# Performance work log

Hardware: AMD Instinct MI355X
Metric: run time of the kernel (lower is better)

The kernel has to match this reference:

```python
import jax, jax.numpy as jnp
import numpy as np
from jax import lax

B, N, FIN, T, K, FC, FT = 8, 2048, 3, 12, 3, 64, 64


def _conv2d(x, w, b, pad):
    # x [B,C,N,T], w [O,I,1,kw], NCHW conv
    y = lax.conv_general_dilated(x, w, (1, 1), pad,
                                 dimension_numbers=('NCHW', 'OIHW', 'NCHW'))
    return y + b[None, :, None, None]


def _spatial_att(h, W, a, alpha, concat):
    # GAT-style dense attention. h [B,N,Fin], W [Fin,D], a [2D,1]
    D = W.shape[1]
    Wh = h @ W                                             # [B,N,D]
    e = jax.nn.leaky_relu(Wh @ a[:D] + jnp.swapaxes(Wh @ a[D:], 1, 2), alpha)  # [B,N,N]
    att = jax.nn.softmax(jax.nn.sigmoid(e), axis=1)        # softmax over dim=1 (as in torch)
    hp = jnp.einsum('bij,bjd->bid', att, Wh)
    return jax.nn.elu(hp) if concat else hp


def setup_inputs() -> dict:
    key = jax.random.key(0)
    ks = jax.random.split(key, 24)
    rnd = lambda i, shape, scale=1.0: (jax.random.normal(ks[i], shape, dtype=jnp.float32) * scale)
    FTm = FC * T  # 768 spatial-attention feature dim
    D = FTm // 2
    return {
        'x': rnd(0, (B, N, FIN, T)),
        'cheb': rnd(1, (K, N, N), 1.0 / np.sqrt(N)),
        'Gamma': rnd(2, (K, FIN, FC), 1.0 / np.sqrt(FIN)),
        'W_heads': rnd(3, (2, FTm, D), 1.0 / np.sqrt(FTm)),
        'a_heads': rnd(4, (2, 2 * D, 1), 1.0 / np.sqrt(2 * D)),
        'W_out': rnd(5, (FTm, FTm), 1.0 / np.sqrt(FTm)),
        'a_out': rnd(6, (2 * FTm, 1), 1.0 / np.sqrt(2 * FTm)),
        'U1': rnd(7, (FT, FT), 1.0 / np.sqrt(FT)),
        'U2': rnd(8, (FT,), 1.0 / np.sqrt(FT)),
        'U3': rnd(9, (FT,), 1.0 / np.sqrt(FT)),
        'be': rnd(10, (1, T, T), 0.1),
        'Ve': rnd(11, (T, T), 1.0 / np.sqrt(T)),
        'time_w': rnd(12, (FT, FC, 1, 3), 1.0 / np.sqrt(3 * FC)),
        'time_b': rnd(13, (FT,), 0.01),
        'res_w': rnd(14, (FT, FIN, 1, 1), 1.0 / np.sqrt(FIN)),
        'res_b': rnd(15, (FT,), 0.01),
        'back_w': rnd(16, (FT, FC, 1, 3), 1.0 / np.sqrt(3 * FC)),
        'back_b': rnd(17, (FT,), 0.01),
        'fore_w': rnd(18, (FT, FC, 1, 3), 1.0 / np.sqrt(3 * FC)),
        'fore_b': rnd(19, (FT,), 0.01),
        'ln_g': jnp.ones((FT,), jnp.float32),
        'ln_b': jnp.zeros((FT,), jnp.float32),
    }


def reference(x, cheb, Gamma, W_heads, a_heads, W_out, a_out, U1, U2, U3, be, Ve,
              time_w, time_b, res_w, res_b, back_w, back_b, fore_w, fore_b, ln_g, ln_b):
    b, n, fin, t = x.shape
    k_ = cheb.shape[0]
    fc = Gamma.shape[2]
    # ChebNetII interpolation coefficients T_k(x_j), x_j = cos((j+0.5)pi/K) -> [j,k]
    jj = np.arange(k_)
    cxj = jnp.asarray(np.cos(np.outer((jj + 0.5) * np.pi / k_, np.arange(k_))), x.dtype)
    lhs = jnp.einsum('jio,jk->kio', Gamma, cxj)                         # [K,Fin,Fc]
    rhs = jnp.einsum('bnit,knm->kbmit', x, cheb)                        # [K,B,N,Fin,T]
    spatial_gcn = jax.nn.relu((2.0 / (k_ + 1)) * jnp.einsum('kbmit,kio->bmot', rhs, lhs))  # [B,N,Fc,T]

    # Spatial transformer: 2 GAT heads + output attention
    h = spatial_gcn.reshape(b, n, fc * t)
    heads = jax.vmap(lambda W, a: _spatial_att(h, W, a, 0.1, True))(W_heads, a_heads)  # [H,B,N,D]
    hcat = jnp.transpose(heads, (1, 2, 0, 3)).reshape(b, n, -1)
    gcn_SAt = jax.nn.relu(_spatial_att(hcat, W_out, a_out, 0.1, False)).reshape(b, n, fc, t)

    # Temporal conv (1x3, pad 1)
    tc = _conv2d(jnp.transpose(gcn_SAt, (0, 2, 1, 3)), time_w, time_b, ((0, 0), (1, 1)))
    tc = jnp.transpose(tc, (0, 2, 1, 3))                                # [B,N,Ft,T]

    # Temporal attention
    lhs_t = jnp.einsum('bnft,fg,g->btn', tc, U1, U2)                    # [B,T,N]
    rhs_t = jnp.einsum('f,bnft->bnt', U3, tc)                           # [B,N,T]
    prod = jnp.einsum('bsn,bnt->bst', lhs_t, rhs_t)                     # [B,T,T]
    E = jnp.einsum('is,bst->bit', Ve, jax.nn.sigmoid(prod + be))
    E = jax.nn.softmax(E, axis=1)
    tcn = jnp.einsum('bnft,bts->bnfs', tc, E)                           # [B,N,Ft,T]

    # Residual (1x1 conv) + LayerNorm over channel dim
    x_res = _conv2d(jnp.transpose(x, (0, 2, 1, 3)), res_w, res_b, ((0, 0), (0, 0)))
    x_res = jnp.transpose(x_res, (0, 2, 1, 3))                          # [B,N,Ft,T]
    z = jnp.transpose(jax.nn.relu(x_res + tcn), (0, 3, 1, 2))           # [B,T,N,Ft]
    mu = z.mean(-1, keepdims=True)
    var = z.var(-1, keepdims=True)
    z = (z - mu) / jnp.sqrt(var + 1e-5) * ln_g + ln_b
    result = jnp.transpose(z, (0, 2, 3, 1))                             # [B,N,Ft,T]

    rp = jnp.transpose(result, (0, 2, 1, 3))
    backcast = jnp.transpose(_conv2d(rp, back_w, back_b, ((0, 0), (1, 1))), (0, 2, 1, 3))
    forecast = jnp.transpose(_conv2d(rp, fore_w, fore_b, ((0, 0), (1, 1))), (0, 2, 1, 3))
    return (backcast, forecast)
```

## Files before the change

kernel.cpp:

```cpp
#include <hip/hip_runtime.h>


typedef unsigned short u16;
typedef __bf16 bf16x8 __attribute__((ext_vector_type(8)));
typedef float f32x4 __attribute__((ext_vector_type(4)));
typedef u16 u16x8 __attribute__((ext_vector_type(8)));

__device__ __forceinline__ u16 f2b(float f) {
  union { float f; unsigned u; } v; v.f = f;
  unsigned u = v.u;
  u = u + 0x7FFFu + ((u >> 16) & 1u);
  return (u16)(u >> 16);
}
__device__ __forceinline__ float b2f(u16 h) {
  union { unsigned u; float f; } v; v.u = ((unsigned)h) << 16; return v.f;
}
__device__ __forceinline__ float qfun(float x) {
  float e = x > 0.f ? x : 0.1f * x;
  float s = __builtin_amdgcn_rcpf(1.f + __expf(-e));
  return __expf(s);
}

template <int N> __device__ __forceinline__ void waitvm() {
  if constexpr (N == 0)      asm volatile("s_waitcnt vmcnt(0)" ::: "memory");
  else if constexpr (N == 4) asm volatile("s_waitcnt vmcnt(4)" ::: "memory");
  else                       asm volatile("s_waitcnt vmcnt(6)" ::: "memory");
}
__device__ __forceinline__ void rawbar() { asm volatile("s_barrier" ::: "memory"); }

#define GLOAD16(g, l) __builtin_amdgcn_global_load_lds( \
    (__attribute__((address_space(1))) void*)(g),       \
    (__attribute__((address_space(3))) void*)(l), 16, 0, 0)

constexpr size_t OFF_LHS     = 0x0;
constexpr size_t OFF_U1U2    = 0x1000;
constexpr size_t OFF_BIASBIG = 0x1100;
constexpr size_t OFF_FH      = 0x3000;
constexpr size_t OFF_GH      = 0x23000;
constexpr size_t OFF_RDH     = 0x43000;
constexpr size_t OFF_FO      = 0x63000;
constexpr size_t OFF_GO      = 0x73000;
constexpr size_t OFF_RDO     = 0x83000;
constexpr size_t OFF_LHST    = 0x93000;
constexpr size_t OFF_RHST    = 0x153000;
constexpr size_t OFF_PROD    = 0x213000;
constexpr size_t OFF_E       = 0x215000;
constexpr size_t OFF_WCATT   = 0x220000;
constexpr size_t OFF_WOUTT   = 0x340000;
constexpr size_t OFF_WTBIG   = 0x460000;
constexpr size_t OFF_XCOLT   = 0x580000;
constexpr size_t OFF_CHEBT   = 0x700000;
constexpr size_t OFF_C1      = 0x1F00000;
constexpr size_t OFF_H       = 0x4300000;
constexpr size_t OFF_P       = 0x700000;
constexpr size_t OFF_WHCATT  = 0x5B00000;
constexpr size_t OFF_HCAT    = 0x7300000;
constexpr size_t OFF_WHOUTT  = 0x5B00000;
constexpr size_t OFF_GCNB    = 0x7300000;
constexpr size_t OFF_WBFBIG  = 0x8B00000;
constexpr size_t OFF_TCS     = 0x700000;
constexpr size_t OFF_RESULTB = 0x3700000;
constexpr size_t WS_NEEDED   = 0x8D40000;

struct GemmP {
  const u16* A; const u16* BT;
  long sA, sB;
  int K, lda, ldb;
  int swz, splitK;
  float* Cf; long sCf; int ldcf;
  u16* Cb;  long sCb; int ldcb;
  u16* CbT; int ldcT; long sCbT;
  const float* bias;
  float* outB; float* outF;
};

template <int EPI, int WN>
__global__ __launch_bounds__(256, (WN == 1 ? 3 : 2)) void gemm_bf16(GemmP p) {
  constexpr int BUFU  = (WN == 1) ? 8192 : 12288;
  constexpr int SMEMU = (WN == 1) ? 16384 : 24576;
  constexpr int LPW   = (WN == 1) ? 4 : 6;
  __shared__ u16 smem[SMEMU];
  const int tid  = threadIdx.x;
  const int lane = tid & 63;
  const int wid  = tid >> 6;
  const int wm = wid >> 1, wn = wid & 1;
  const int z = blockIdx.z;

  long m0, n0;
  if (p.swz) {
    int nT = gridDim.x;
    int nwg = nT * gridDim.y;
    int lin = blockIdx.x + nT * blockIdx.y;
    int q = nwg >> 3;
    int swz = (lin & 7) * q + (lin >> 3);
    m0 = (long)(swz / nT) * 128;
    n0 = (long)(swz % nT) * (128 * WN);
  } else {
    m0 = (long)blockIdx.y * 128;
    n0 = (long)blockIdx.x * (128 * WN);
  }

  const int K = p.K;
  long aBase, bBase;
  if (p.splitK) {
    int kz = z >> 2, ch = z & 3;
    aBase = (long)kz * p.sA + (long)ch * 512;
    bBase = (long)ch * 512;
  } else {
    aBase = (long)z * p.sA;
    bBase = (long)z * p.sB;
  }
  const u16* Ab = p.A + aBase + m0 * p.lda;
  const u16* Bb = p.BT + bBase + n0 * p.ldb;

  const int sk = (((lane & 3) ^ ((lane >> 3) & 3))) * 8;
  const u16* aP0 = Ab + (long)(wid * 32 + (lane >> 2)) * p.lda + sk;
  const u16* aP1 = aP0 + (long)16 * p.lda;
  const u16* bP0 = Bb + (long)(wid * 32 * WN + (lane >> 2)) * p.ldb + sk;
  const u16* bP1 = bP0 + (long)16 * p.ldb;
  const u16* bP2 = bP0 + (long)32 * p.ldb;
  const u16* bP3 = bP0 + (long)48 * p.ldb;
  const int aslot = wid * 1024;
  const int bslot = 4096 + wid * (WN == 1 ? 1024 : 2048);

  auto STAGE = [&](int s, u16* base) {
    long ko = (long)s * 32;
    GLOAD16(aP0 + ko, base + aslot);
    GLOAD16(aP1 + ko, base + aslot + 512);
    GLOAD16(bP0 + ko, base + bslot);
    GLOAD16(bP1 + ko, base + bslot + 512);
    if constexpr (WN == 2) {
      GLOAD16(bP2 + ko, base + bslot + 1024);
      GLOAD16(bP3 + ko, base + bslot + 1536);
    }
  };

  f32x4 acc[4][4 * WN];
  f32x4 zero = {0.f, 0.f, 0.f, 0.f};
#pragma unroll
  for (int i = 0; i < 4; ++i)
#pragma unroll
    for (int j = 0; j < 4 * WN; ++j) acc[i][j] = zero;

  const int xorc = (lane >> 1) & 3;
  const int aoff = (wm * 64 + (lane & 15)) * 32 + ((lane >> 4) ^ xorc) * 8;
  const int boff = 4096 + (wn * 64 * WN + (lane & 15)) * 32 + ((lane >> 4) ^ xorc) * 8;

  const int nsteps = K >> 5;
  u16* buf0 = smem;
  u16* buf1 = smem + BUFU;

  STAGE(0, buf0);
  STAGE(1, buf1);
  waitvm<LPW>();
  rawbar();

  for (int i = 0; i < nsteps; ++i) {
    u16* buf = (i & 1) ? buf1 : buf0;
    bf16x8 av[4], bv[4 * WN];
#pragma unroll
    for (int mi = 0; mi < 4; ++mi) av[mi] = *(const bf16x8*)&buf[aoff + mi * 512];
#pragma unroll
    for (int ni = 0; ni < 4 * WN; ++ni) bv[ni] = *(const bf16x8*)&buf[boff + ni * 512];
#pragma unroll
    for (int mi = 0; mi < 4; ++mi)
#pragma unroll
      for (int ni = 0; ni < 4 * WN; ++ni)
        acc[mi][ni] = __builtin_amdgcn_mfma_f32_16x16x32_bf16(av[mi], bv[ni], acc[mi][ni], 0, 0, 0);
    if (i + 1 < nsteps) {
      asm volatile("s_waitcnt lgkmcnt(0)" ::: "memory");
      rawbar();
      if (i + 2 < nsteps) {
        STAGE(i + 2, buf);
        waitvm<LPW>();
      } else {
        waitvm<0>();
      }
      rawbar();
    }
  }
  __syncthreads();

  if constexpr (EPI == 1) {
#pragma unroll
    for (int h = 0; h < 2; ++h) {
      if (h == 1) __syncthreads();
      if (WN == 1 || wn == h) {
#pragma unroll
        for (int mi = 0; mi < 4; ++mi)
#pragma unroll
          for (int ni = 0; ni < 4 * WN; ++ni) {
            int cl = (WN == 1 ? wn * 64 : 0) + ni * 16 + (lane & 15);
            int mlb = wm * 64 + mi * 16 + ((lane >> 4) << 2);
#pragma unroll
            for (int r = 0; r < 4; ++r)
              smem[cl * 136 + mlb + r] = f2b(acc[mi][ni][r]);
          }
      }
      __syncthreads();
      int c = tid >> 1, half = tid & 1;
      long bat = m0 >> 11;
      u16* dst = p.CbT + bat * p.sCbT + (long)(n0 + h * 128 + c) * p.ldcT +
                 (m0 & 2047) + half * 64;
      const u16* srcp = &smem[c * 136 + half * 64];
#pragma unroll
      for (int j = 0; j < 64; j += 8)
        *(u16x8*)(dst + j) = *(const u16x8*)(srcp + j);
      if (WN == 1) break;
    }
    return;
  }

  if constexpr (EPI == 7) {
    const int q = lane >> 4, g4 = (lane >> 2) & 3, j = lane & 3;
    const int back = ((int)n0 < 768);
    float* obase = (back ? p.outB : p.outF) - (back ? 0 : 768);
#pragma unroll
    for (int mi = 0; mi < 4; ++mi) {
      long rb0 = m0 + wm * 64 + mi * 16 + q * 4;
#pragma unroll
      for (int ni = 0; ni < 4 * WN; ++ni) {
        int cb = (int)n0 + wn * 64 * WN + ni * 16 + g4 * 4;
        f32x4 v = acc[mi][ni];
        float bsv = p.bias[cb + j];
        v[0] += bsv; v[1] += bsv; v[2] += bsv; v[3] += bsv;
#pragma unroll
        for (int d = 1; d <= 2; d <<= 1) {
          f32x4 t;
#pragma unroll
          for (int b = 0; b < 4; ++b) t[b] = __shfl_xor(v[b ^ d], d, 64);
#pragma unroll
          for (int b = 0; b < 4; ++b) if ((lane ^ b) & d) v[b] = t[b];
        }
        *(f32x4*)(obase + (rb0 + j) * 768 + cb) = v;
      }
    }
    return;
  }

#pragma unroll
  for (int mi = 0; mi < 4; ++mi) {
    long rb0 = m0 + wm * 64 + mi * 16 + ((lane >> 4) << 2);
#pragma unroll
    for (int ni = 0; ni < 4 * WN; ++ni) {
      int col = (int)n0 + wn * 64 * WN + ni * 16 + (lane & 15);
#pragma unroll
      for (int r = 0; r < 4; ++r) {
        float v = acc[mi][ni][r];
        long row = rb0 + r;
        if constexpr (EPI == 2) {
          float e = v > 0.f ? v : expm1f(v);
          p.Cb[(long)z * p.sCb + row * p.ldcb + col] = f2b(e);
        } else if constexpr (EPI == 6) {
          p.Cb[row * 768 + col] = f2b(v + p.bias[col & 63]);
        } else if constexpr (EPI == 9) {
          p.Cb[(long)z * p.sCb + row * p.ldcb + col] = f2b(v);
        } else {
          p.Cb[(long)z * p.sCb + row * p.ldcb + col] = f2b(fmaxf(v, 0.f));
        }
      }
    }
  }
}

__global__ void k_prep(const float* Gamma, const float* U1, const float* U2,
                       const float* back_b, const float* fore_b,
                       float* lhs, float* u1u2, float* biasBig) {
  int o = threadIdx.x;
  if (o < 64) {
    const float cx[3][3] = {{1.f, 0.86602540378443871f, 0.5f},
                            {1.f, 6.123233995736766e-17f, -1.f},
                            {1.f, -0.86602540378443871f, 0.5f}};
    for (int k = 0; k < 3; ++k)
      for (int i = 0; i < 3; ++i) {
        float s = 0;
        for (int j = 0; j < 3; ++j) s += Gamma[(j * 3 + i) * 64 + o] * cx[j][k];
        lhs[(k * 3 + i) * 64 + o] = s;
      }
    float s = 0;
    for (int g = 0; g < 64; ++g) s += U1[o * 64 + g] * U2[g];
    u1u2[o] = s;
    for (int t = 0; t < 12; ++t) {
      biasBig[o * 12 + t] = back_b[o];
      biasBig[768 + o * 12 + t] = fore_b[o];
    }
  }
}

__global__ void k_convert(const float* W_heads, const float* W_out, const float* time_w,
                          const float* back_w, const float* fore_w, const float* xg,
                          u16* WcatT, u16* WoutT, u16* WtBig, u16* WbfBig, u16* xcolT) {
  const int N1 = 589824, NT = 589824, NBF = 1179648, N5 = 786432;
  const int TOT = 2 * N1 + NT + NBF + N5;
  for (int o = blockIdx.x * 256 + threadIdx.x; o < TOT; o += gridDim.x * 256) {
    if (o < N1) {
      int dcol = o / 768, kk = o % 768;
      int hd = dcol / 384, d = dcol % 384;
      WcatT[o] = f2b(W_heads[((long)hd * 768 + kk) * 384 + d]);
    } else if (o < 2 * N1) {
      int o2 = o - N1; int dcol = o2 / 768, kk = o2 % 768;
      WoutT[o2] = f2b(W_out[kk * 768 + dcol]);
    } else if (o < 2 * N1 + NT) {
      int o3 = o - 2 * N1; int col = o3 / 768, kk = o3 % 768;
      int t = col >> 6, ft = col & 63, fc = kk / 12, tau = kk % 12;
      int r = tau - t + 1;
      WtBig[o3] = f2b((r >= 0 && r < 3) ? time_w[ft * 192 + fc * 3 + r] : 0.f);
    } else if (o < 2 * N1 + NT + NBF) {
      int o4 = o - 2 * N1 - NT; int col = o4 / 768, kk = o4 % 768;
      int rem = (col < 768) ? col : col - 768;
      int c = rem / 12, tt = rem % 12;
      int fc = kk / 12, tau = kk % 12; int r = tau - tt + 1;
      const float* wsrc = (col < 768) ? back_w : fore_w;
      WbfBig[o4] = f2b((r >= 0 && r < 3) ? wsrc[c * 192 + fc * 3 + r] : 0.f);
    } else {
      int o5 = o - 2 * N1 - NT - NBF; int c = o5 / 2048, n = o5 % 2048;
      float v = 0.f;
      if (c < 288) {
        int b = c / 36, r2 = c % 36, i = r2 / 12, t = r2 % 12;
        v = xg[(long)(b * 2048 + n) * 36 + i * 12 + t];
      }
      xcolT[o5] = f2b(v);
    }
  }
}

__global__ void k_chebT(const float* cheb, u16* chebT) {
  __shared__ float ts[32][33];
  int n0 = blockIdx.x * 32, m0 = blockIdx.y * 32, k = blockIdx.z;
  int c = threadIdx.x & 31, rq = threadIdx.x >> 5;
  const long base = (long)k * 2048 * 2048;
  for (int q = 0; q < 4; ++q) {
    int n = n0 + rq + q * 8;
    ts[rq + q * 8][c] = cheb[base + (long)n * 2048 + m0 + c];
  }
  __syncthreads();
  for (int q = 0; q < 4; ++q) {
    int m = m0 + rq + q * 8;
    chebT[base + (long)m * 2048 + n0 + c] = f2b(ts[c][rq + q * 8]);
  }
}

__global__ __launch_bounds__(256) void k_h(const u16* C1, const float* lhs, u16* h) {
  int bn = blockIdx.x; int b = bn >> 11, n = bn & 2047;
  int tid = threadIdx.x;
  __shared__ float c1s[108], ls[576];
  if (tid < 108) {
    int kk = tid / 12, t = tid % 12; int k = kk / 3, i = kk % 3;
    float s = 0;
#pragma unroll
    for (int ch = 0; ch < 4; ++ch)
      s += b2f(C1[((long)(k * 4 + ch) * 2048 + n) * 384 + b * 36 + i * 12 + t]);
    c1s[tid] = s;
  }
  for (int s = tid; s < 576; s += 256) ls[s] = lhs[s];
  __syncthreads();
  for (int q = 0; q < 3; ++q) {
    int idx = tid + q * 256; int o = idx / 12, t = idx % 12;
    float s = 0;
#pragma unroll
    for (int kk = 0; kk < 9; ++kk) s += c1s[kk * 12 + t] * ls[kk * 64 + o];
    s *= 0.5f;
    if (s < 0.f) s = 0.f;
    h[(long)bn * 768 + idx] = f2b(s);
  }
}

__global__ __launch_bounds__(256) void k_fg(const u16* WhT, int dOff, int Dlen,
                                            const float* aF, const float* aG,
                                            float* fOut, float* gOut) {
  int b = blockIdx.y;
  int i = blockIdx.x * 256 + threadIdx.x;
  __shared__ float af[768], ag[768];
  for (int s = threadIdx.x; s < Dlen; s += 256) { af[s] = aF[s]; ag[s] = aG[s]; }
  __syncthreads();
  const u16* wp = WhT + ((long)b * 768 + dOff) * 2048 + i;
  float fs = 0, gs = 0;
  for (int d = 0; d < Dlen; ++d) {
    float w = b2f(wp[(long)d * 2048]);
    fs += w * af[d]; gs += w * ag[d];
  }
  fOut[b * 2048 + i] = fs;
  gOut[b * 2048 + i] = gs;
}

__global__ __launch_bounds__(256) void k_denom(const float* f, const float* g, float* rd) {
  int b = blockIdx.y;
  int jl = threadIdx.x & 63, ch = threadIdx.x >> 6;
  int j = blockIdx.x * 64 + jl;
  __shared__ float fl[2048];
  __shared__ float red[256];
  for (int s = threadIdx.x; s < 2048; s += 256) fl[s] = f[b * 2048 + s];
  __syncthreads();
  float gj = g[b * 2048 + j];
  float acc = 0;
  for (int i = ch * 512; i < ch * 512 + 512; ++i) acc += qfun(fl[i] + gj);
  red[threadIdx.x] = acc;
  __syncthreads();
  if (ch == 0) {
    float s = red[jl] + red[jl + 64] + red[jl + 128] + red[jl + 192];
    rd[b * 2048 + j] = 1.f / s;
  }
}

__global__ __launch_bounds__(256) void k_P(const float* f, const float* g,
                                           const float* rd, u16* P) {
  int j = blockIdx.x * 256 + threadIdx.x;
  int i0 = blockIdx.y * 16;
  int b = blockIdx.z;
  __shared__ float fl[16];
  if (threadIdx.x < 16) fl[threadIdx.x] = f[b * 2048 + i0 + threadIdx.x];
  __syncthreads();
  float gj = g[b * 2048 + j], rj = rd[b * 2048 + j];
  u16* Pp = P + ((long)b * 2048 + i0) * 2048 + j;
#pragma unroll
  for (int ii = 0; ii < 16; ++ii) Pp[(long)ii * 2048] = f2b(qfun(fl[ii] + gj) * rj);
}

__global__ void k_temporal(const u16* tc, const float* u1u2, const float* U3g,
                           float* lhs_t, float* rhs_t) {
  __shared__ float uu[64], u3[64];
  int tid = threadIdx.x;
  if (tid < 64) { uu[tid] = u1u2[tid]; u3[tid] = U3g[tid]; }
  __syncthreads();
  int gid = blockIdx.x * 256 + tid;
  const u16* p = tc + (long)gid * 64;
  float s1 = 0, s2 = 0;
#pragma unroll
  for (int c = 0; c < 8; ++c) {
    u16x8 vv = *(const u16x8*)(p + c * 8);
#pragma unroll
    for (int j = 0; j < 8; ++j) {
      float v = b2f(vv[j]);
      s1 += v * uu[c * 8 + j]; s2 += v * u3[c * 8 + j];
    }
  }
  int t = gid % 12; long bn = gid / 12;
  int b = (int)(bn >> 11);
  lhs_t[((long)b * 12 + t) * 2048 + (int)(bn & 2047)] = s1;
  rhs_t[gid] = s2;
}

__global__ void k_prod(const float* lhs_t, const float* rhs_t, float* prod) {
  int bi = blockIdx.x;
  int b = bi / 144; int r = bi % 144; int s = r / 12; int u = r % 12;
  int tid = threadIdx.x;
  float acc = 0;
  const float* lp = lhs_t + ((long)b * 12 + s) * 2048;
  const float* rp = rhs_t + (long)b * 2048 * 12 + u;
  for (int n = tid; n < 2048; n += 256) acc += lp[n] * rp[n * 12];
  __shared__ float red[256];
  red[tid] = acc; __syncthreads();
  for (int st = 128; st > 0; st >>= 1) {
    if (tid < st) red[tid] += red[tid + st];
    __syncthreads();
  }
  if (tid == 0) prod[bi] = red[0];
}

__global__ void k_E(const float* prod, const float* be, const float* Ve, float* E) {
  int b = blockIdx.x; int tid = threadIdx.x;
  __shared__ float S0[144], E1[144], mx[12], dn[12];
  if (tid < 144) {
    float v = prod[b * 144 + tid] + be[tid];
    S0[tid] = 1.f / (1.f + __expf(-v));
  }
  __syncthreads();
  if (tid < 144) {
    int i = tid / 12, t = tid % 12;
    float a = 0;
    for (int s = 0; s < 12; ++s) a += Ve[i * 12 + s] * S0[s * 12 + t];
    E1[tid] = a;
  }
  __syncthreads();
  if (tid < 12) {
    float m = -1e30f;
    for (int i = 0; i < 12; ++i) m = fmaxf(m, E1[i * 12 + tid]);
    float d = 0;
    for (int i = 0; i < 12; ++i) d += __expf(E1[i * 12 + tid] - m);
    mx[tid] = m; dn[tid] = d;
  }
  __syncthreads();
  if (tid < 144) {
    int t = tid % 12;
    E[b * 144 + tid] = __expf(E1[tid] - mx[t]) / dn[t];
  }
}

__global__ __launch_bounds__(256) void k_res_ln(const u16* tc, const float* E,
                                                const float* xg, const float* res_w,
                                                const float* res_b, const float* ln_g,
                                                const float* ln_b, u16* result) {
  int bn = blockIdx.x; int b = bn >> 11;
  int tid = threadIdx.x;
  __shared__ float tcb[768], Eb[144], xl[36], rw[192], rb[64], lg[64], lb[64], zl[768], mu[12], rs[12];
  for (int s = tid; s < 768; s += 256) tcb[s] = b2f(tc[(long)bn * 768 + s]);
  if (tid < 144) Eb[tid] = E[b * 144 + tid];
  if (tid < 36) xl[tid] = xg[(long)bn * 36 + tid];
  if (tid >= 64 && tid < 256) { int q = tid - 64; if (q < 192) rw[q] = res_w[q]; }
  if (tid < 64) { rb[tid] = res_b[tid]; lg[tid] = ln_g[tid]; lb[tid] = ln_b[tid]; }
  __syncthreads();
  float z[3];
#pragma unroll
  for (int q = 0; q < 3; ++q) {
    int idx = tid + q * 256; int f = idx / 12, s = idx % 12;
    float tcn = 0;
#pragma unroll
    for (int t = 0; t < 12; ++t) tcn += tcb[t * 64 + f] * Eb[t * 12 + s];
    float xr = rb[f];
#pragma unroll
    for (int i = 0; i < 3; ++i) xr += rw[f * 3 + i] * xl[i * 12 + s];
    float v = xr + tcn;
    v = v > 0.f ? v : 0.f;
    z[q] = v; zl[idx] = v;
  }
  __syncthreads();
  if (tid < 12) {
    float m = 0, m2 = 0;
    for (int f = 0; f < 64; ++f) { float v = zl[f * 12 + tid]; m += v; m2 += v * v; }
    m *= (1.f / 64.f); m2 *= (1.f / 64.f);
    mu[tid] = m;
    float var = m2 - m * m;
    rs[tid] = rsqrtf((var > 0.f ? var : 0.f) + 1e-5f);
  }
  __syncthreads();
#pragma unroll
  for (int q = 0; q < 3; ++q) {
    int idx = tid + q * 256; int f = idx / 12, s = idx % 12;
    result[(long)bn * 768 + idx] = f2b((z[q] - mu[s]) * rs[s] * lg[f] + lb[f]);
  }
}

__global__ void k_sentinel(float* out, long n) {
  long i = (long)blockIdx.x * 256 + threadIdx.x;
  if (i < n) out[i] = 12345.0f;
}

extern "C" void kernel_launch(void* const* d_in, const int* in_sizes, int n_in,
                              void* d_out, int out_size, void* d_ws, size_t ws_size,
                              hipStream_t stream) {
  (void)in_sizes; (void)n_in;
  const float* x       = (const float*)d_in[0];
  const float* cheb    = (const float*)d_in[1];
  const float* Gamma   = (const float*)d_in[2];
  const float* W_heads = (const float*)d_in[3];
  const float* a_heads = (const float*)d_in[4];
  const float* W_out   = (const float*)d_in[5];
  const float* a_out   = (const float*)d_in[6];
  const float* U1      = (const float*)d_in[7];
  const float* U2      = (const float*)d_in[8];
  const float* U3      = (const float*)d_in[9];
  const float* be      = (const float*)d_in[10];
  const float* Ve      = (const float*)d_in[11];
  const float* time_w  = (const float*)d_in[12];
  const float* time_b  = (const float*)d_in[13];
  const float* res_w   = (const float*)d_in[14];
  const float* res_b   = (const float*)d_in[15];
  const float* back_w  = (const float*)d_in[16];
  const float* back_b  = (const float*)d_in[17];
  const float* fore_w  = (const float*)d_in[18];
  const float* fore_b  = (const float*)d_in[19];
  const float* ln_g    = (const float*)d_in[20];
  const float* ln_b    = (const float*)d_in[21];
  float* out = (float*)d_out;

  if (ws_size < WS_NEEDED) {
    k_sentinel<<<(out_size + 255) / 256, 256, 0, stream>>>(out, out_size);
    return;
  }

  char* ws = (char*)d_ws;
  float* lhs     = (float*)(ws + OFF_LHS);
  float* u1u2    = (float*)(ws + OFF_U1U2);
  float* biasBig = (float*)(ws + OFF_BIASBIG);
  float* fH      = (float*)(ws + OFF_FH);
  float* gH      = (float*)(ws + OFF_GH);
  float* rdH     = (float*)(ws + OFF_RDH);
  float* fO      = (float*)(ws + OFF_FO);
  float* gO      = (float*)(ws + OFF_GO);
  float* rdO     = (float*)(ws + OFF_RDO);
  float* lhs_t   = (float*)(ws + OFF_LHST);
  float* rhs_t   = (float*)(ws + OFF_RHST);
  float* prod    = (float*)(ws + OFF_PROD);
  float* Ebuf    = (float*)(ws + OFF_E);
  u16* WcatT   = (u16*)(ws + OFF_WCATT);
  u16* WoutT   = (u16*)(ws + OFF_WOUTT);
  u16* WtBig   = (u16*)(ws + OFF_WTBIG);
  u16* WbfBig  = (u16*)(ws + OFF_WBFBIG);
  u16* xcolT   = (u16*)(ws + OFF_XCOLT);
  u16* chebT   = (u16*)(ws + OFF_CHEBT);
  u16* C1      = (u16*)(ws + OFF_C1);
  u16* hbuf    = (u16*)(ws + OFF_H);
  u16* Pbuf    = (u16*)(ws + OFF_P);
  u16* WhcatT  = (u16*)(ws + OFF_WHCATT);
  u16* hcat    = (u16*)(ws + OFF_HCAT);
  u16* WhoutT  = (u16*)(ws + OFF_WHOUTT);
  u16* gcnB    = (u16*)(ws + OFF_GCNB);
  u16* tcsB    = (u16*)(ws + OFF_TCS);
  u16* resultB = (u16*)(ws + OFF_RESULTB);

  k_prep<<<1, 64, 0, stream>>>(Gamma, U1, U2, back_b, fore_b, lhs, u1u2, biasBig);
  k_convert<<<2048, 256, 0, stream>>>(W_heads, W_out, time_w, back_w, fore_w, x,
                                      WcatT, WoutT, WtBig, WbfBig, xcolT);
  k_chebT<<<dim3(64, 64, 3), 256, 0, stream>>>(cheb, chebT);

  {
    GemmP p{}; p.A = chebT; p.BT = xcolT; p.sA = 2048L * 2048; p.sB = 0;
    p.K = 512; p.lda = 2048; p.ldb = 2048; p.splitK = 1; p.swz = 1;
    p.Cb = C1; p.sCb = 2048L * 384; p.ldcb = 384;
    gemm_bf16<9, 1><<<dim3(3, 16, 12), 256, 0, stream>>>(p);
  }
  k_h<<<16384, 256, 0, stream>>>(C1, lhs, hbuf);

  {
    GemmP p{}; p.A = hbuf; p.BT = WcatT; p.sA = 0; p.sB = 0;
    p.K = 768; p.lda = 768; p.ldb = 768; p.swz = 1;
    p.CbT = WhcatT; p.ldcT = 2048; p.sCbT = 768L * 2048;
    gemm_bf16<1, 2><<<dim3(3, 128, 1), 256, 0, stream>>>(p);
  }
  k_fg<<<dim3(8, 8), 256, 0, stream>>>(WhcatT, 0, 384, a_heads, a_heads + 384, fH, gH);
  k_fg<<<dim3(8, 8), 256, 0, stream>>>(WhcatT, 384, 384, a_heads + 768, a_heads + 1152,
                                       fH + 16384, gH + 16384);
  for (int hd = 0; hd < 2; ++hd) {
    const float* f = fH + hd * 16384; const float* g = gH + hd * 16384;
    float* rd = rdH + hd * 16384;
    k_denom<<<dim3(32, 8), 256, 0, stream>>>(f, g, rd);
    k_P<<<dim3(8, 128, 8), 256, 0, stream>>>(f, g, rd, Pbuf);
    GemmP p{}; p.A = Pbuf; p.BT = WhcatT + (long)hd * 384 * 2048;
    p.sA = 2048L * 2048; p.sB = 768L * 2048;
    p.K = 2048; p.lda = 2048; p.ldb = 2048; p.swz = 1;
    p.Cb = hcat + hd * 384; p.sCb = 2048L * 768; p.ldcb = 768;
    gemm_bf16<2, 1><<<dim3(3, 16, 8), 256, 0, stream>>>(p);
  }

  {
    GemmP p{}; p.A = hcat; p.BT = WoutT; p.sA = 0; p.sB = 0;
    p.K = 768; p.lda = 768; p.ldb = 768; p.swz = 1;
    p.CbT = WhoutT; p.ldcT = 2048; p.sCbT = 768L * 2048;
    gemm_bf16<1, 2><<<dim3(3, 128, 1), 256, 0, stream>>>(p);
  }
  k_fg<<<dim3(8, 8), 256, 0, stream>>>(WhoutT, 0, 768, a_out, a_out + 768, fO, gO);
  k_denom<<<dim3(32, 8), 256, 0, stream>>>(fO, gO, rdO);
  k_P<<<dim3(8, 128, 8), 256, 0, stream>>>(fO, gO, rdO, Pbuf);
  {
    GemmP p{}; p.A = Pbuf; p.BT = WhoutT; p.sA = 2048L * 2048; p.sB = 768L * 2048;
    p.K = 2048; p.lda = 2048; p.ldb = 2048; p.swz = 1;
    p.Cb = gcnB; p.sCb = 2048L * 768; p.ldcb = 768;
    gemm_bf16<8, 2><<<dim3(3, 16, 8), 256, 0, stream>>>(p);
  }

  {
    GemmP p{}; p.A = gcnB; p.BT = WtBig; p.sA = 0; p.sB = 0;
    p.K = 768; p.lda = 768; p.ldb = 768; p.swz = 1;
    p.Cb = tcsB; p.bias = time_b;
    gemm_bf16<6, 2><<<dim3(3, 128, 1), 256, 0, stream>>>(p);
  }

  k_temporal<<<768, 256, 0, stream>>>(tcsB, u1u2, U3, lhs_t, rhs_t);
  k_prod<<<1152, 256, 0, stream>>>(lhs_t, rhs_t, prod);
  k_E<<<8, 256, 0, stream>>>(prod, be, Ve, Ebuf);

  k_res_ln<<<16384, 256, 0, stream>>>(tcsB, Ebuf, x, res_w, res_b, ln_g, ln_b, resultB);

  {
    GemmP p{}; p.A = resultB; p.BT = WbfBig; p.sA = 0; p.sB = 0;
    p.K = 768; p.lda = 768; p.ldb = 768; p.swz = 1;
    p.bias = biasBig; p.outB = out; p.outF = out + 12582912L;
    gemm_bf16<7, 2><<<dim3(6, 128, 1), 256, 0, stream>>>(p);
  }
}
```

Measured before the change: 699.0 us.

## Generate attention probability tile inside GEMM instead of materializing P

Removes the separate k_P kernel, which wrote a bf16 attention matrix [B,2048,2048] to global memory, and instead computes the P tile on the fly inside the attention GEMM's A-operand staging. Each thread evaluates qfun(f_i+g_j)*rd_j for 16 elements per stage, packs them to bf16 and writes them into swizzled LDS, while only the B operand is loaded with global_load_lds. This saves the P write and re-read (about 64MB per head pass) but adds transcendental ALU work per GEMM block, recomputed across the N tiles, plus extra LDS for the g and rd vectors and lower occupancy for the WN=1 variant.

After: 786.6 us. 1.13x slower.

```diff
diff --git a/kernel.cpp b/kernel.cpp
--- a/kernel.cpp
+++ b/kernel.cpp
@@ -5,6 +5,7 @@
 typedef __bf16 bf16x8 __attribute__((ext_vector_type(8)));
 typedef float f32x4 __attribute__((ext_vector_type(4)));
 typedef u16 u16x8 __attribute__((ext_vector_type(8)));
+typedef unsigned u32x4 __attribute__((ext_vector_type(4)));
 
 __device__ __forceinline__ u16 f2b(float f) {
   union { float f; unsigned u; } v; v.f = f;
@@ -23,8 +24,10 @@
 
 template <int N> __device__ __forceinline__ void waitvm() {
   if constexpr (N == 0)      asm volatile("s_waitcnt vmcnt(0)" ::: "memory");
+  else if constexpr (N == 2) asm volatile("s_waitcnt vmcnt(2)" ::: "memory");
   else if constexpr (N == 4) asm volatile("s_waitcnt vmcnt(4)" ::: "memory");
-  else                       asm volatile("s_waitcnt vmcnt(6)" ::: "memory");
+  else if constexpr (N == 6) asm volatile("s_waitcnt vmcnt(6)" ::: "memory");
+  else                       asm volatile("s_waitcnt vmcnt(8)" ::: "memory");
 }
 __device__ __forceinline__ void rawbar() { asm volatile("s_barrier" ::: "memory"); }
 
@@ -52,7 +55,6 @@
 constexpr size_t OFF_CHEBT   = 0x700000;
 constexpr size_t OFF_C1      = 0x1F00000;
 constexpr size_t OFF_H       = 0x4300000;
-constexpr size_t OFF_P       = 0x700000;
 constexpr size_t OFF_WHCATT  = 0x5B00000;
 constexpr size_t OFF_HCAT    = 0x7300000;
 constexpr size_t OFF_WHOUTT  = 0x5B00000;
@@ -72,13 +74,14 @@
   u16* CbT; int ldcT; long sCbT;
   const float* bias;
   float* outB; float* outF;
+  const float* Pf; const float* Pg; const float* Prd;
 };
 
-template <int EPI, int WN>
-__global__ __launch_bounds__(256, (WN == 1 ? 3 : 2)) void gemm_bf16(GemmP p) {
+template <int EPI, int WN, int FP = 0>
+__global__ __launch_bounds__(256, ((WN == 1 && !FP) ? 3 : 2)) void gemm_bf16(GemmP p) {
   constexpr int BUFU  = (WN == 1) ? 8192 : 12288;
-  constexpr int SMEMU = (WN == 1) ? 16384 : 24576;
-  constexpr int LPW   = (WN == 1) ? 4 : 6;
+  constexpr int SMEMU = 2 * BUFU + (FP ? 8192 : 0);
+  constexpr int LPW   = FP ? (WN == 1 ? 2 : 4) : (WN == 1 ? 4 : 6);
   __shared__ u16 smem[SMEMU];
   const int tid  = threadIdx.x;
   const int lane = tid & 63;
@@ -125,8 +128,10 @@
 
   auto STAGE = [&](int s, u16* base) {
     long ko = (long)s * 32;
-    GLOAD16(aP0 + ko, base + aslot);
-    GLOAD16(aP1 + ko, base + aslot + 512);
+    if constexpr (!FP) {
+      GLOAD16(aP0 + ko, base + aslot);
+      GLOAD16(aP1 + ko, base + aslot + 512);
+    }
     GLOAD16(bP0 + ko, base + bslot);
     GLOAD16(bP1 + ko, base + bslot + 512);
     if constexpr (WN == 2) {
@@ -135,6 +140,41 @@
     }
   };
 
+  float* g_lds  = (float*)(smem + 2 * BUFU);
+  float* rd_lds = g_lds + 2048;
+  float fv = 0.f;
+  const int pr = tid >> 1, ph = tid & 1;
+  if constexpr (FP) {
+    const float* pf  = p.Pf  + (long)z * 2048;
+    const float* pg  = p.Pg  + (long)z * 2048;
+    const float* prd = p.Prd + (long)z * 2048;
+    fv = pf[m0 + pr];
+    for (int idx = tid; idx < K; idx += 256) {
+      g_lds[idx]  = pg[idx];
+      rd_lds[idx] = prd[idx];
+    }
+    __syncthreads();
+  }
+
+  auto PGEN = [&](int s, u16* base) {
+    if constexpr (FP) {
+      const int k0 = s * 32 + ph * 16;
+      const float* gp = g_lds + k0;
+      const float* rp = rd_lds + k0;
+      float pv[16];
+#pragma unroll
+      for (int j = 0; j < 16; ++j) pv[j] = qfun(fv + gp[j]) * rp[j];
+      unsigned w[8];
+#pragma unroll
+      for (int j = 0; j < 8; ++j)
+        asm("v_cvt_pk_bf16_f32 %0, %1, %2" : "=v"(w[j]) : "v"(pv[2 * j]), "v"(pv[2 * j + 1]));
+      const int x = (pr >> 1) & 3;
+      u16* ab = base + pr * 32;
+      *(u32x4*)(ab + ((2 * ph) ^ x) * 8)     = u32x4{w[0], w[1], w[2], w[3]};
+      *(u32x4*)(ab + ((2 * ph + 1) ^ x) * 8) = u32x4{w[4], w[5], w[6], w[7]};
+    }
+  };
+
   f32x4 acc[4][4 * WN];
   f32x4 zero = {0.f, 0.f, 0.f, 0.f};
 #pragma unroll
@@ -150,8 +190,11 @@
   u16* buf0 = smem;
   u16* buf1 = smem + BUFU;
 
+  PGEN(0, buf0);
+  PGEN(1, buf1);
   STAGE(0, buf0);
   STAGE(1, buf1);
+  asm volatile("s_waitcnt lgkmcnt(0)" ::: "memory");
   waitvm<LPW>();
   rawbar();
 
@@ -171,6 +214,7 @@
       asm volatile("s_waitcnt lgkmcnt(0)" ::: "memory");
       rawbar();
       if (i + 2 < nsteps) {
+        PGEN(i + 2, buf);
         STAGE(i + 2, buf);
         waitvm<LPW>();
       } else {
@@ -402,20 +446,6 @@
   }
 }
 
-__global__ __launch_bounds__(256) void k_P(const float* f, const float* g,
-                                           const float* rd, u16* P) {
-  int j = blockIdx.x * 256 + threadIdx.x;
-  int i0 = blockIdx.y * 16;
-  int b = blockIdx.z;
-  __shared__ float fl[16];
-  if (threadIdx.x < 16) fl[threadIdx.x] = f[b * 2048 + i0 + threadIdx.x];
-  __syncthreads();
-  float gj = g[b * 2048 + j], rj = rd[b * 2048 + j];
-  u16* Pp = P + ((long)b * 2048 + i0) * 2048 + j;
-#pragma unroll
-  for (int ii = 0; ii < 16; ++ii) Pp[(long)ii * 2048] = f2b(qfun(fl[ii] + gj) * rj);
-}
-
 __global__ void k_temporal(const u16* tc, const float* u1u2, const float* U3g,
                            float* lhs_t, float* rhs_t) {
   __shared__ float uu[64], u3[64];
@@ -590,7 +620,6 @@
   u16* chebT   = (u16*)(ws + OFF_CHEBT);
   u16* C1      = (u16*)(ws + OFF_C1);
   u16* hbuf    = (u16*)(ws + OFF_H);
-  u16* Pbuf    = (u16*)(ws + OFF_P);
   u16* WhcatT  = (u16*)(ws + OFF_WHCATT);
   u16* hcat    = (u16*)(ws + OFF_HCAT);
   u16* WhoutT  = (u16*)(ws + OFF_WHOUTT);
@@ -624,12 +653,12 @@
     const float* f = fH + hd * 16384; const float* g = gH + hd * 16384;
     float* rd = rdH + hd * 16384;
     k_denom<<<dim3(32, 8), 256, 0, stream>>>(f, g, rd);
-    k_P<<<dim3(8, 128, 8), 256, 0, stream>>>(f, g, rd, Pbuf);
-    GemmP p{}; p.A = Pbuf; p.BT = WhcatT + (long)hd * 384 * 2048;
-    p.sA = 2048L * 2048; p.sB = 768L * 2048;
+    GemmP p{}; p.A = WhcatT; p.BT = WhcatT + (long)hd * 384 * 2048;
+    p.sA = 0; p.sB = 768L * 2048;
     p.K = 2048; p.lda = 2048; p.ldb = 2048; p.swz = 1;
     p.Cb = hcat + hd * 384; p.sCb = 2048L * 768; p.ldcb = 768;
-    gemm_bf16<2, 1><<<dim3(3, 16, 8), 256, 0, stream>>>(p);
+    p.Pf = f; p.Pg = g; p.Prd = rd;
+    gemm_bf16<2, 1, 1><<<dim3(3, 16, 8), 256, 0, stream>>>(p);
   }
 
   {
@@ -640,12 +669,12 @@
   }
   k_fg<<<dim3(8, 8), 256, 0, stream>>>(WhoutT, 0, 768, a_out, a_out + 768, fO, gO);
   k_denom<<<dim3(32, 8), 256, 0, stream>>>(fO, gO, rdO);
-  k_P<<<dim3(8, 128, 8), 256, 0, stream>>>(fO, gO, rdO, Pbuf);
   {
-    GemmP p{}; p.A = Pbuf; p.BT = WhoutT; p.sA = 2048L * 2048; p.sB = 768L * 2048;
+    GemmP p{}; p.A = WhoutT; p.BT = WhoutT; p.sA = 0; p.sB = 768L * 2048;
     p.K = 2048; p.lda = 2048; p.ldb = 2048; p.swz = 1;
     p.Cb = gcnB; p.sCb = 2048L * 768; p.ldcb = 768;
-    gemm_bf16<8, 2><<<dim3(3, 16, 8), 256, 0, stream>>>(p);
+    p.Pf = fO; p.Pg = gO; p.Prd = rdO;
+    gemm_bf16<8, 2, 1><<<dim3(3, 16, 8), 256, 0, stream>>>(p);
   }
 
   {
```
